# Optimization experiments

Measured on AMD Instinct MI355X. Metric: run time of the kernel, lower is better.

Reference implementation:

```python
import jax, jax.numpy as jnp
import numpy as np

B, H, S, DK = 2, 16, 2048, 64
NEG = jnp.float32(-10000.0)


def setup_inputs() -> dict:
    key = jax.random.key(0)
    kq, kk, kv, km = jax.random.split(key, 4)
    query = jax.random.normal(kq, (B, H, S, DK), dtype=jnp.float32)
    k_ = jax.random.normal(kk, (B, H, S, DK), dtype=jnp.float32)
    value = jax.random.normal(kv, (B, H, S, DK), dtype=jnp.float32)
    mask = (jax.random.uniform(km, (B, 1, S, S)) > 0.5).astype(jnp.float32)
    return {"query": query, "key": k_, "value": value, "mask": mask, "d_k": DK}


def reference(query, key, value, mask, d_k):
    # scores: [B,H,S,S]
    scale = jnp.float32(1.0 / np.sqrt(d_k))
    scores = jnp.einsum('bhqd,bhkd->bhqk', query, key) * scale * mask
    # non-standard masking: keep only strictly positive masked scores
    scores = jnp.where(scores > 0, scores, NEG)
    attn = jax.nn.softmax(scores, axis=-1)
    return jnp.einsum('bhqk,bhkd->bhqd', attn, value)
```

## Files before the change

### kernel.cpp

```cpp
#include <hip/hip_runtime.h>
#include <hip/hip_bf16.h>
#include <math.h>

#define S_LEN 2048
#define D_KV  64
#define BQ    128
#define BK    64
#define LP    72
#define NIT   (S_LEN / BK)
#define KVS   (64 * LP)

typedef __attribute__((ext_vector_type(8)))  short    bh8;
typedef __attribute__((ext_vector_type(4)))  short    sh4;
typedef __attribute__((ext_vector_type(4)))  unsigned ux4;
typedef __attribute__((ext_vector_type(16))) float    f32x16;

__device__ __forceinline__ short f2bf(float f) {
    unsigned u = __builtin_bit_cast(unsigned, f);
    u += 0x7fffu + ((u >> 16) & 1u);
    return (short)(u >> 16);
}
__device__ __forceinline__ unsigned pk2(float a, float b) {
    return (unsigned)(unsigned short)f2bf(a) |
           ((unsigned)(unsigned short)f2bf(b) << 16);
}
__device__ __forceinline__ void lds_barrier() {
    asm volatile("s_waitcnt lgkmcnt(0)\n\ts_barrier" ::: "memory");
}

__global__ __launch_bounds__(256, 2)
void attn_fwd(const float* __restrict__ Qg, const float* __restrict__ Kg,
              const float* __restrict__ Vg, const float* __restrict__ Mg,
              float* __restrict__ Og)
{
    __shared__ __align__(16) short smem[4 * KVS];

    const int tid  = threadIdx.x;
    const int wave = tid >> 6;
    const int lane = tid & 63;
    const int n    = lane & 31;
    const int hi   = lane >> 5;

    const int qt = blockIdx.x;
    const int bh = blockIdx.y;
    const int b  = bh >> 4;

    const int qw = qt * BQ + wave * 32;

    const float* Qp = Qg + ((size_t)bh * S_LEN + qw) * D_KV;
    const float* Kp = Kg + (size_t)bh * S_LEN * D_KV;
    const float* Vp = Vg + (size_t)bh * S_LEN * D_KV;
    const float* Mp = Mg + (size_t)b * S_LEN * S_LEN;
    float*       Op = Og + ((size_t)bh * S_LEN + qw) * D_KV;

    bh8 qf[4];
#pragma unroll
    for (int kc = 0; kc < 4; ++kc) {
        const float* src = Qp + n * D_KV + kc * 16 + hi * 8;
        float4 a0 = *(const float4*)(src);
        float4 a1 = *(const float4*)(src + 4);
        bh8 f;
        f[0] = f2bf(a0.x * 0.125f); f[1] = f2bf(a0.y * 0.125f);
        f[2] = f2bf(a0.z * 0.125f); f[3] = f2bf(a0.w * 0.125f);
        f[4] = f2bf(a1.x * 0.125f); f[5] = f2bf(a1.y * 0.125f);
        f[6] = f2bf(a1.z * 0.125f); f[7] = f2bf(a1.w * 0.125f);
        qf[kc] = f;
    }

    f32x16 o0, o1;
    float  l = 0.f;
#pragma unroll
    for (int i = 0; i < 16; ++i) { o0[i] = 0.f; o1[i] = 0.f; }

    float4 kreg[4], vreg[4], mreg[8];

    auto load_kv = [&](int kt) {
#pragma unroll
        for (int i = 0; i < 4; ++i) {
            int idx = tid + 256 * i;
            int kr  = idx >> 4;
            int db  = (idx & 15) * 4;
            kreg[i] = *(const float4*)(Kp + (size_t)(kt + kr) * D_KV + db);
        }
#pragma unroll
        for (int i = 0; i < 4; ++i) {
            int db = wave * 16 + i * 4;
            vreg[i] = *(const float4*)(Vp + (size_t)(kt + lane) * D_KV + db);
        }
    };
    auto load_mask = [&](int kt) {
        const float* mrow = Mp + (size_t)(qw + n) * S_LEN + kt + 4 * hi;
#pragma unroll
        for (int mg = 0; mg < 4; ++mg) {
            mreg[2 * mg]     = *(const float4*)(mrow + mg * 8);
            mreg[2 * mg + 1] = *(const float4*)(mrow + 32 + mg * 8);
        }
    };
    auto write_stage = [&](int pb) {
        short* kl = smem + pb * KVS;
        short* vl = smem + (2 + pb) * KVS;
#pragma unroll
        for (int i = 0; i < 4; ++i) {
            int idx = tid + 256 * i;
            int kr  = idx >> 4;
            int db  = (idx & 15) * 4;
            sh4 s4;
            s4[0] = f2bf(kreg[i].x); s4[1] = f2bf(kreg[i].y);
            s4[2] = f2bf(kreg[i].z); s4[3] = f2bf(kreg[i].w);
            *(sh4*)&kl[kr * LP + db] = s4;
        }
#pragma unroll
        for (int i = 0; i < 4; ++i) {
            int db = wave * 16 + i * 4;
            vl[(db + 0) * LP + lane] = f2bf(vreg[i].x);
            vl[(db + 1) * LP + lane] = f2bf(vreg[i].y);
            vl[(db + 2) * LP + lane] = f2bf(vreg[i].z);
            vl[(db + 3) * LP + lane] = f2bf(vreg[i].w);
        }
    };

    load_kv(0);
    write_stage(0);
    load_kv(BK);
    load_mask(0);
    lds_barrier();

    for (int j = 0; j < NIT; ++j) {
        const int pb = j & 1;
        const short* kl = smem + pb * KVS;
        const short* vl = smem + (2 + pb) * KVS;

        f32x16 s0, s1;
#pragma unroll
        for (int i = 0; i < 16; ++i) { s0[i] = 0.f; s1[i] = 0.f; }
#pragma unroll
        for (int kc = 0; kc < 4; ++kc) {
            int off = kc * 16 + hi * 8;
            bh8 kf0 = *(const bh8*)&kl[n * LP + off];
            bh8 kf1 = *(const bh8*)&kl[(32 + n) * LP + off];
            s0 = __builtin_amdgcn_mfma_f32_32x32x16_bf16(kf0, qf[kc], s0, 0, 0, 0);
            s1 = __builtin_amdgcn_mfma_f32_32x32x16_bf16(kf1, qf[kc], s1, 0, 0, 0);
        }

        if (j < NIT - 1) write_stage(pb ^ 1);
        if (j < NIT - 2) load_kv((j + 2) * BK);

        unsigned pk0[8], pk1[8];
#pragma unroll
        for (int mg = 0; mg < 4; ++mg) {
            float4 m0 = mreg[2 * mg];
            float4 m1 = mreg[2 * mg + 1];
            float ma[4] = {m0.x, m0.y, m0.z, m0.w};
            float mb[4] = {m1.x, m1.y, m1.z, m1.w};
            float p0[4], p1[4];
#pragma unroll
            for (int x = 0; x < 4; ++x) {
                int r = 4 * mg + x;
                float t0 = s0[r] * ma[x];
                float t1 = s1[r] * mb[x];
                p0[x] = (t0 > 0.f) ? __expf(t0) : 0.f;
                p1[x] = (t1 > 0.f) ? __expf(t1) : 0.f;
                l += p0[x] + p1[x];
            }
            pk0[2 * mg]     = pk2(p0[0], p0[1]);
            pk0[2 * mg + 1] = pk2(p0[2], p0[3]);
            pk1[2 * mg]     = pk2(p1[0], p1[1]);
            pk1[2 * mg + 1] = pk2(p1[2], p1[3]);
        }
        if (j < NIT - 1) load_mask((j + 1) * BK);

#pragma unroll
        for (int kc = 0; kc < 4; ++kc) {
            const unsigned* pk = (kc < 2) ? pk0 : pk1;
            int kk = kc & 1;
            unsigned X0 = hi ? pk[4 * kk]     : pk[4 * kk + 2];
            unsigned X1 = hi ? pk[4 * kk + 1] : pk[4 * kk + 3];
            unsigned Y0 = (unsigned)__shfl_xor((int)X0, 32);
            unsigned Y1 = (unsigned)__shfl_xor((int)X1, 32);
            ux4 bb;
            if (hi) { bb[0] = Y0; bb[1] = Y1; bb[2] = pk[4 * kk + 2]; bb[3] = pk[4 * kk + 3]; }
            else    { bb[0] = pk[4 * kk]; bb[1] = pk[4 * kk + 1]; bb[2] = Y0; bb[3] = Y1; }
            bh8 pb8 = __builtin_bit_cast(bh8, bb);
            int off = kc * 16 + hi * 8;
            bh8 vf0 = *(const bh8*)&vl[n * LP + off];
            bh8 vf1 = *(const bh8*)&vl[(32 + n) * LP + off];
            o0 = __builtin_amdgcn_mfma_f32_32x32x16_bf16(vf0, pb8, o0, 0, 0, 0);
            o1 = __builtin_amdgcn_mfma_f32_32x32x16_bf16(vf1, pb8, o1, 0, 0, 0);
        }

        if (j < NIT - 1) lds_barrier();
    }

    l += __shfl_xor(l, 32);
    float inv = 1.0f / l;
    float* orow = Op + (size_t)n * D_KV;
#pragma unroll
    for (int mg = 0; mg < 4; ++mg) {
        int d0 = 8 * mg + 4 * hi;
        float4 a = {o0[4 * mg] * inv, o0[4 * mg + 1] * inv,
                    o0[4 * mg + 2] * inv, o0[4 * mg + 3] * inv};
        float4 c = {o1[4 * mg] * inv, o1[4 * mg + 1] * inv,
                    o1[4 * mg + 2] * inv, o1[4 * mg + 3] * inv};
        *(float4*)(orow + d0)      = a;
        *(float4*)(orow + 32 + d0) = c;
    }
}

extern "C" void kernel_launch(void* const* d_in, const int* in_sizes, int n_in,
                              void* d_out, int out_size, void* d_ws, size_t ws_size,
                              hipStream_t stream) {
    const float* Q = (const float*)d_in[0];
    const float* K = (const float*)d_in[1];
    const float* V = (const float*)d_in[2];
    const float* M = (const float*)d_in[3];
    float*       O = (float*)d_out;
    dim3 grid(S_LEN / BQ, 32);
    attn_fwd<<<grid, 256, 0, stream>>>(Q, K, V, M, O);
}
```

Baseline: 204.5 us.

## Pre-convert K/V to bf16 fragment layout and stream via global_load_lds

Two new pre-pass kernels convert K and V to bf16 and store them in the exact per-lane MFMA fragment order in workspace memory. The attention kernel then copies each 64-key tile straight from global memory into LDS with global_load_lds, double-buffered two tiles ahead. This removes the per-block fp32 loads, bf16 conversion and transposing LDS stores. The mask registers are also double-buffered so the next tile's mask loads are issued earlier. The cost is two extra kernel launches plus extra workspace writes and reads.

```diff
diff --git a/kernel.cpp b/kernel.cpp
--- a/kernel.cpp
+++ b/kernel.cpp
@@ -6,12 +6,12 @@
 #define D_KV  64
 #define BQ    128
 #define BK    64
-#define LP    72
 #define NIT   (S_LEN / BK)
-#define KVS   (64 * LP)
+#define CHUNK 512
+#define KTILE_SHORTS (8 * CHUNK)
+#define PREP_UNITS (32 * 32 * 4 * 2 * 64)
 
 typedef __attribute__((ext_vector_type(8)))  short    bh8;
-typedef __attribute__((ext_vector_type(4)))  short    sh4;
 typedef __attribute__((ext_vector_type(4)))  unsigned ux4;
 typedef __attribute__((ext_vector_type(16))) float    f32x16;
 
@@ -24,16 +24,50 @@
     return (unsigned)(unsigned short)f2bf(a) |
            ((unsigned)(unsigned short)f2bf(b) << 16);
 }
-__device__ __forceinline__ void lds_barrier() {
-    asm volatile("s_waitcnt lgkmcnt(0)\n\ts_barrier" ::: "memory");
+__device__ __forceinline__ void glds16(const short* g, short* l) {
+    __builtin_amdgcn_global_load_lds(
+        (const __attribute__((address_space(1))) unsigned*)g,
+        (__attribute__((address_space(3))) unsigned*)l, 16, 0, 0);
+}
+
+__global__ void prep_k(const float* __restrict__ K, short* __restrict__ Kf) {
+    int g   = blockIdx.x * 256 + threadIdx.x;
+    int lam = g & 63, n = lam & 31, hi = lam >> 5;
+    int q   = (g >> 6) & 1;
+    int kc  = (g >> 7) & 3;
+    int kt  = (g >> 9) & 31;
+    int bh  = g >> 14;
+    const float* src = K + ((size_t)bh * S_LEN + kt * 64 + q * 32 + n) * D_KV
+                         + kc * 16 + hi * 8;
+    float4 a0 = *(const float4*)src;
+    float4 a1 = *(const float4*)(src + 4);
+    bh8 f;
+    f[0] = f2bf(a0.x); f[1] = f2bf(a0.y); f[2] = f2bf(a0.z); f[3] = f2bf(a0.w);
+    f[4] = f2bf(a1.x); f[5] = f2bf(a1.y); f[6] = f2bf(a1.z); f[7] = f2bf(a1.w);
+    *(bh8*)(Kf + (size_t)g * 8) = f;
+}
+
+__global__ void prep_v(const float* __restrict__ V, short* __restrict__ Vf) {
+    int g   = blockIdx.x * 256 + threadIdx.x;
+    int lam = g & 63, n = lam & 31, hi = lam >> 5;
+    int u   = (g >> 6) & 1;
+    int kc  = (g >> 7) & 3;
+    int kt  = (g >> 9) & 31;
+    int bh  = g >> 14;
+    const float* src = V + ((size_t)bh * S_LEN + kt * 64 + kc * 16 + hi * 8) * D_KV
+                         + u * 32 + n;
+    bh8 f;
+#pragma unroll
+    for (int e = 0; e < 8; ++e) f[e] = f2bf(src[(size_t)e * D_KV]);
+    *(bh8*)(Vf + (size_t)g * 8) = f;
 }
 
 __global__ __launch_bounds__(256, 2)
-void attn_fwd(const float* __restrict__ Qg, const float* __restrict__ Kg,
-              const float* __restrict__ Vg, const float* __restrict__ Mg,
+void attn_fwd(const float* __restrict__ Qg, const short* __restrict__ Kf,
+              const short* __restrict__ Vf, const float* __restrict__ Mg,
               float* __restrict__ Og)
 {
-    __shared__ __align__(16) short smem[4 * KVS];
+    __shared__ __align__(16) short smem[2 * 2 * KTILE_SHORTS];
 
     const int tid  = threadIdx.x;
     const int wave = tid >> 6;
@@ -47,11 +81,11 @@
 
     const int qw = qt * BQ + wave * 32;
 
-    const float* Qp = Qg + ((size_t)bh * S_LEN + qw) * D_KV;
-    const float* Kp = Kg + (size_t)bh * S_LEN * D_KV;
-    const float* Vp = Vg + (size_t)bh * S_LEN * D_KV;
-    const float* Mp = Mg + (size_t)b * S_LEN * S_LEN;
-    float*       Op = Og + ((size_t)bh * S_LEN + qw) * D_KV;
+    const float* Qp  = Qg + ((size_t)bh * S_LEN + qw) * D_KV;
+    const short* Kfb = Kf + (size_t)bh * (NIT * KTILE_SHORTS);
+    const short* Vfb = Vf + (size_t)bh * (NIT * KTILE_SHORTS);
+    const float* Mp  = Mg + (size_t)b * S_LEN * S_LEN;
+    float*       Op  = Og + ((size_t)bh * S_LEN + qw) * D_KV;
 
     bh8 qf[4];
 #pragma unroll
@@ -72,92 +106,59 @@
 #pragma unroll
     for (int i = 0; i < 16; ++i) { o0[i] = 0.f; o1[i] = 0.f; }
 
-    float4 kreg[4], vreg[4], mreg[8];
-
-    auto load_kv = [&](int kt) {
-#pragma unroll
-        for (int i = 0; i < 4; ++i) {
-            int idx = tid + 256 * i;
-            int kr  = idx >> 4;
-            int db  = (idx & 15) * 4;
-            kreg[i] = *(const float4*)(Kp + (size_t)(kt + kr) * D_KV + db);
-        }
-#pragma unroll
-        for (int i = 0; i < 4; ++i) {
-            int db = wave * 16 + i * 4;
-            vreg[i] = *(const float4*)(Vp + (size_t)(kt + lane) * D_KV + db);
+    float4 mreg[2][8];
+
+    auto stage = [&](int kt, int pb) {
+        const short* gk = Kfb + (size_t)kt * KTILE_SHORTS;
+        const short* gv = Vfb + (size_t)kt * KTILE_SHORTS;
+        short* lk = &smem[pb * 2 * KTILE_SHORTS];
+        short* lv = lk + KTILE_SHORTS;
+#pragma unroll
+        for (int i = 0; i < 2; ++i) {
+            int idx = wave + 4 * i;
+            glds16(gk + idx * CHUNK + lane * 8, lk + idx * CHUNK);
+            glds16(gv + idx * CHUNK + lane * 8, lv + idx * CHUNK);
         }
     };
-    auto load_mask = [&](int kt) {
+    auto load_mask = [&](int kt, int mb) {
         const float* mrow = Mp + (size_t)(qw + n) * S_LEN + kt + 4 * hi;
 #pragma unroll
         for (int mg = 0; mg < 4; ++mg) {
-            mreg[2 * mg]     = *(const float4*)(mrow + mg * 8);
-            mreg[2 * mg + 1] = *(const float4*)(mrow + 32 + mg * 8);
+            mreg[mb][2 * mg]     = *(const float4*)(mrow + mg * 8);
+            mreg[mb][2 * mg + 1] = *(const float4*)(mrow + 32 + mg * 8);
         }
     };
-    auto write_stage = [&](int pb) {
-        short* kl = smem + pb * KVS;
-        short* vl = smem + (2 + pb) * KVS;
-#pragma unroll
-        for (int i = 0; i < 4; ++i) {
-            int idx = tid + 256 * i;
-            int kr  = idx >> 4;
-            int db  = (idx & 15) * 4;
-            sh4 s4;
-            s4[0] = f2bf(kreg[i].x); s4[1] = f2bf(kreg[i].y);
-            s4[2] = f2bf(kreg[i].z); s4[3] = f2bf(kreg[i].w);
-            *(sh4*)&kl[kr * LP + db] = s4;
-        }
-#pragma unroll
-        for (int i = 0; i < 4; ++i) {
-            int db = wave * 16 + i * 4;
-            vl[(db + 0) * LP + lane] = f2bf(vreg[i].x);
-            vl[(db + 1) * LP + lane] = f2bf(vreg[i].y);
-            vl[(db + 2) * LP + lane] = f2bf(vreg[i].z);
-            vl[(db + 3) * LP + lane] = f2bf(vreg[i].w);
-        }
-    };
-
-    load_kv(0);
-    write_stage(0);
-    load_kv(BK);
-    load_mask(0);
-    lds_barrier();
-
-    for (int j = 0; j < NIT; ++j) {
-        const int pb = j & 1;
-        const short* kl = smem + pb * KVS;
-        const short* vl = smem + (2 + pb) * KVS;
+
+    auto body = [&](int j, int pb) {
+        const short* lk = &smem[pb * 2 * KTILE_SHORTS];
+        const short* lv = lk + KTILE_SHORTS;
+
+        if (j + 1 < NIT) load_mask((j + 1) * BK, pb ^ 1);
 
         f32x16 s0, s1;
 #pragma unroll
         for (int i = 0; i < 16; ++i) { s0[i] = 0.f; s1[i] = 0.f; }
 #pragma unroll
         for (int kc = 0; kc < 4; ++kc) {
-            int off = kc * 16 + hi * 8;
-            bh8 kf0 = *(const bh8*)&kl[n * LP + off];
-            bh8 kf1 = *(const bh8*)&kl[(32 + n) * LP + off];
+            bh8 kf0 = *(const bh8*)&lk[(kc * 2 + 0) * CHUNK + lane * 8];
+            bh8 kf1 = *(const bh8*)&lk[(kc * 2 + 1) * CHUNK + lane * 8];
             s0 = __builtin_amdgcn_mfma_f32_32x32x16_bf16(kf0, qf[kc], s0, 0, 0, 0);
             s1 = __builtin_amdgcn_mfma_f32_32x32x16_bf16(kf1, qf[kc], s1, 0, 0, 0);
         }
 
-        if (j < NIT - 1) write_stage(pb ^ 1);
-        if (j < NIT - 2) load_kv((j + 2) * BK);
-
         unsigned pk0[8], pk1[8];
 #pragma unroll
         for (int mg = 0; mg < 4; ++mg) {
-            float4 m0 = mreg[2 * mg];
-            float4 m1 = mreg[2 * mg + 1];
+            float4 m0 = mreg[pb][2 * mg];
+            float4 m1 = mreg[pb][2 * mg + 1];
             float ma[4] = {m0.x, m0.y, m0.z, m0.w};
-            float mb[4] = {m1.x, m1.y, m1.z, m1.w};
+            float mb4[4] = {m1.x, m1.y, m1.z, m1.w};
             float p0[4], p1[4];
 #pragma unroll
             for (int x = 0; x < 4; ++x) {
                 int r = 4 * mg + x;
                 float t0 = s0[r] * ma[x];
-                float t1 = s1[r] * mb[x];
+                float t1 = s1[r] * mb4[x];
                 p0[x] = (t0 > 0.f) ? __expf(t0) : 0.f;
                 p1[x] = (t1 > 0.f) ? __expf(t1) : 0.f;
                 l += p0[x] + p1[x];
@@ -167,7 +168,6 @@
             pk1[2 * mg]     = pk2(p1[0], p1[1]);
             pk1[2 * mg + 1] = pk2(p1[2], p1[3]);
         }
-        if (j < NIT - 1) load_mask((j + 1) * BK);
 
 #pragma unroll
         for (int kc = 0; kc < 4; ++kc) {
@@ -181,14 +181,24 @@
             if (hi) { bb[0] = Y0; bb[1] = Y1; bb[2] = pk[4 * kk + 2]; bb[3] = pk[4 * kk + 3]; }
             else    { bb[0] = pk[4 * kk]; bb[1] = pk[4 * kk + 1]; bb[2] = Y0; bb[3] = Y1; }
             bh8 pb8 = __builtin_bit_cast(bh8, bb);
-            int off = kc * 16 + hi * 8;
-            bh8 vf0 = *(const bh8*)&vl[n * LP + off];
-            bh8 vf1 = *(const bh8*)&vl[(32 + n) * LP + off];
+            bh8 vf0 = *(const bh8*)&lv[(kc * 2 + 0) * CHUNK + lane * 8];
+            bh8 vf1 = *(const bh8*)&lv[(kc * 2 + 1) * CHUNK + lane * 8];
             o0 = __builtin_amdgcn_mfma_f32_32x32x16_bf16(vf0, pb8, o0, 0, 0, 0);
             o1 = __builtin_amdgcn_mfma_f32_32x32x16_bf16(vf1, pb8, o1, 0, 0, 0);
         }
 
-        if (j < NIT - 1) lds_barrier();
+        __syncthreads();
+        if (j + 2 < NIT) stage(j + 2, pb);
+    };
+
+    stage(0, 0);
+    stage(1, 1);
+    load_mask(0, 0);
+    __syncthreads();
+
+    for (int jj = 0; jj < NIT; jj += 2) {
+        body(jj, 0);
+        body(jj + 1, 1);
     }
 
     l += __shfl_xor(l, 32);
@@ -214,6 +224,13 @@
     const float* V = (const float*)d_in[2];
     const float* M = (const float*)d_in[3];
     float*       O = (float*)d_out;
+
+    short* Kf = (short*)d_ws;
+    short* Vf = Kf + (size_t)PREP_UNITS * 8;
+
+    prep_k<<<PREP_UNITS / 256, 256, 0, stream>>>(K, Kf);
+    prep_v<<<PREP_UNITS / 256, 256, 0, stream>>>(V, Vf);
+
     dim3 grid(S_LEN / BQ, 32);
-    attn_fwd<<<grid, 256, 0, stream>>>(Q, K, V, M, O);
-}
+    attn_fwd<<<grid, 256, 0, stream>>>(Q, Kf, Vf, M, O);
+}
```

Result: no change. 203.7 us (-0.4%).
